# Kernel optimization log

Hardware: AMD Instinct MI355X
Metric: run time of the kernel (lower is better)

## Reference

```python
import jax, jax.numpy as jnp
import numpy as np
import math

D_MODEL = 512
NUM_HEADS = 8
B, L = 2, 4096
EPS_NORM = 1e-8
PLASTICITY = 1.0


def setup_inputs() -> dict:
    key = jax.random.key(0)
    ks = jax.random.split(key, 6)
    D, H = D_MODEL, NUM_HEADS
    std = 1.0 / math.sqrt(D)
    x = jax.random.normal(ks[0], (B, L, D), dtype=jnp.float32)
    qkv_w = jax.random.normal(ks[1], (3 * D, D), dtype=jnp.float32) * std
    qkv_b = jnp.zeros((3 * D,), dtype=jnp.float32)
    out_w = jax.random.normal(ks[2], (D, D), dtype=jnp.float32) * std
    out_b = jnp.zeros((D,), dtype=jnp.float32)
    decay_w = jax.random.normal(ks[3], (H, D), dtype=jnp.float32) * 0.02
    decay_b = jnp.full((H,), 4.0, dtype=jnp.float32)
    norm_scale = jnp.ones((D,), dtype=jnp.float32)
    return {"x": x, "qkv_w": qkv_w, "qkv_b": qkv_b, "out_w": out_w,
            "out_b": out_b, "decay_w": decay_w, "decay_b": decay_b,
            "norm_scale": norm_scale}


def _hebbian_forward(x, qkv_w, qkv_b, out_w, out_b, decay_w, decay_b, norm_scale):
    Bsz, Lsz, D = x.shape
    H = NUM_HEADS
    E = D // H
    # QKV projection (torch Linear: y = x @ W.T + b)
    qkv = x @ qkv_w.T + qkv_b
    q, k, v = jnp.split(qkv, 3, axis=-1)
    q = q.reshape(Bsz, Lsz, H, E)
    k = k.reshape(Bsz, Lsz, H, E)
    v = v.reshape(Bsz, Lsz, H, E)
    # feature map: elu(x) + 1
    q = (jax.nn.elu(q) + 1.0) / math.sqrt(E)
    k = jax.nn.elu(k) + 1.0
    # input-dependent decay per head
    decay_logits = x @ decay_w.T + decay_b          # (B,L,H)
    lambdas = (0.9 + 0.1 * jax.nn.sigmoid(decay_logits)) * PLASTICITY
    log_lambdas = jnp.log(jnp.clip(lambdas, 1e-6))[..., None]   # (B,L,H,1)
    log_lambda_cum = jnp.clip(jnp.cumsum(log_lambdas, axis=1), -50.0, 50.0)
    decay_k = jnp.exp(-log_lambda_cum)
    decay_q = jnp.exp(log_lambda_cum)
    k_decayed = k * decay_k
    q_decayed = q * decay_q
    # outer-product memory state cumsum: (B,L,H,E,E)
    kv = jnp.einsum('blhe,blhf->blhef', k_decayed, v)
    memory_state = jnp.cumsum(kv, axis=1)
    k_sum_decayed = jnp.cumsum(k_decayed, axis=1)
    num = jnp.einsum('blhe,blhef->blhf', q_decayed, memory_state)
    den = jnp.einsum('blhe,blhe->blh', q_decayed, k_sum_decayed)[..., None] + 1e-6
    out = (num / den).reshape(Bsz, Lsz, D)
    out = out @ out_w.T + out_b
    # RMSNorm (dropout is identity in eval)
    rnorm = jax.lax.rsqrt(jnp.mean(out * out, axis=-1, keepdims=True) + EPS_NORM)
    return out * rnorm * norm_scale


def reference(x, qkv_w, qkv_b, out_w, out_b, decay_w, decay_b, norm_scale):
    return _hebbian_forward(x, qkv_w, qkv_b, out_w, out_b, decay_w, decay_b, norm_scale)
```

## Files before the change

### kernel.cpp

```cpp
#include <hip/hip_runtime.h>

typedef unsigned short u16;
typedef unsigned int u32;

#define B_ 2
#define L_ 4096
#define D_ 512
#define H_ 8
#define E_ 64
#define M_ (B_*L_)
#define TD (3*D_)
#define NCH (L_/64)
#define BH (B_*H_)

typedef short bf16x8 __attribute__((ext_vector_type(8)));
typedef float f32x4 __attribute__((ext_vector_type(4)));

__device__ __forceinline__ float bf2f(u16 u){ return __uint_as_float(((u32)u)<<16); }
__device__ __forceinline__ u16 f2bf(float f){
  u32 u = __float_as_uint(f);
  u32 r = u + 0x7FFFu + ((u>>16)&1u);
  return (u16)(r>>16);
}
__device__ __forceinline__ float elu1(float v){ return v>0.f ? v+1.f : __expf(v); }

__device__ __forceinline__ void async_ld16(const u16* g, u16* l){
  __builtin_amdgcn_global_load_lds(
      (const __attribute__((address_space(1))) void*)g,
      (__attribute__((address_space(3))) void*)l, 16, 0, 0);
}

__global__ __launch_bounds__(256) void decay_conv_kernel(const float* __restrict__ x,
    const float* __restrict__ dw, const float* __restrict__ db,
    const float* __restrict__ qw, const float* __restrict__ ow,
    float* __restrict__ ll, u16* __restrict__ xb,
    u16* __restrict__ qwb, u16* __restrict__ owb)
{
  int blk = blockIdx.x;
  if (blk < 2048){
    int wv = threadIdx.x>>6, lane = threadIdx.x&63;
    int m = blk*4 + wv;
    float xr[8];
    #pragma unroll
    for (int i=0;i<8;i++) xr[i] = x[(size_t)m*D_ + lane + 64*i];
    #pragma unroll
    for (int i=0;i<8;i++) xb[(size_t)m*D_ + lane + 64*i] = f2bf(xr[i]);
    int b = m >> 12, l = m & (L_-1);
    float acc8[8];
    #pragma unroll
    for (int h=0; h<8; h++){
      float a = 0.f;
      #pragma unroll
      for (int i=0;i<8;i++) a += xr[i]*dw[h*D_ + lane + 64*i];
      acc8[h] = a;
    }
    float s4[4];
    #pragma unroll
    for (int i=0;i<4;i++){
      float a = acc8[2*i], bb = acc8[2*i+1];
      bool odd = lane & 1;
      float keep = odd ? bb : a;
      float send = odd ? a : bb;
      s4[i] = keep + __shfl_xor(send, 1);
    }
    float s2[2];
    #pragma unroll
    for (int j=0;j<2;j++){
      float a = s4[2*j], bb = s4[2*j+1];
      bool sel = (lane>>1) & 1;
      float keep = sel ? bb : a;
      float send = sel ? a : bb;
      s2[j] = keep + __shfl_xor(send, 2);
    }
    float r;
    {
      bool sel = (lane>>2) & 1;
      float keep = sel ? s2[1] : s2[0];
      float send = sel ? s2[0] : s2[1];
      r = keep + __shfl_xor(send, 4);
    }
    r += __shfl_xor(r, 8);
    r += __shfl_xor(r, 16);
    r += __shfl_xor(r, 32);
    if (lane < 8){
      float z = r + db[lane];
      float lam = 0.9f + 0.1f/(1.f + __expf(-z));
      ll[((b*H_+lane)*L_) + l] = __logf(lam);
    }
  } else {
    int gid = (blk-2048)*256 + threadIdx.x;
    const float* src; u16* dst; int off;
    if (gid < 196608){ src = qw; dst = qwb; off = gid; }
    else { src = ow; dst = owb; off = gid - 196608; }
    float4 v = ((const float4*)src)[off];
    ushort4 o; o.x=f2bf(v.x); o.y=f2bf(v.y); o.z=f2bf(v.z); o.w=f2bf(v.w);
    ((ushort4*)dst)[off] = o;
  }
}

__global__ __launch_bounds__(256) void scan_kernel(const float* __restrict__ ll,
    float* __restrict__ cb)
{
  int bh = blockIdx.x, t = threadIdx.x;
  int lane = t & 63, wv = t >> 6;
  const float* p = ll + (size_t)bh*L_ + t*16;
  float s[16];
  #pragma unroll
  for (int q=0;q<4;q++){
    float4 v = *(const float4*)(p + q*4);
    s[q*4+0]=v.x; s[q*4+1]=v.y; s[q*4+2]=v.z; s[q*4+3]=v.w;
  }
  #pragma unroll
  for (int i=1;i<16;i++) s[i] += s[i-1];
  float tot = s[15];
  float ws = tot;
  #pragma unroll
  for (int off=1; off<64; off<<=1){
    float tmp = __shfl_up(ws, off);
    if (lane >= off) ws += tmp;
  }
  __shared__ float wsum[4];
  if (lane == 63) wsum[wv] = ws;
  __syncthreads();
  float base = 0.f;
  #pragma unroll
  for (int w2=0; w2<3; w2++) if (w2 < wv) base += wsum[w2];
  float ex = base + ws - tot;
  float* c = cb + (size_t)bh*L_ + t*16;
  #pragma unroll
  for (int i=0;i<16;i++) c[i] = fminf(50.f, fmaxf(-50.f, ex + s[i]));
}

template<bool OB>
__global__ __launch_bounds__(256) void gemm_mfma(const u16* __restrict__ A,
    const u16* __restrict__ W, const float* __restrict__ bias,
    void* __restrict__ Cv, int M, int N, int K)
{
  __shared__ u16 As[2][128*32];
  __shared__ u16 Bs[2][128*32];
  int n0 = blockIdx.x*128, m0 = blockIdx.y*128;
  int t = threadIdx.x, wave = t>>6, lane = t&63;
  int wm = (wave>>1)*64, wn = (wave&1)*64;
  f32x4 acc[4][4] = {};
  int srow = wave*32 + (lane>>2);
  int scol = (lane&3)*8;
  const u16* gA = A + (size_t)(m0+srow)*K + scol;
  const u16* gB = W + (size_t)(n0+srow)*K + scol;
  int q8 = (lane>>4)*8, r16 = lane&15;
  {
    u16* lA = As[0] + wave*1024;
    u16* lB = Bs[0] + wave*1024;
    async_ld16(gA,                lA);
    async_ld16(gA + 16*(size_t)K, lA + 512);
    async_ld16(gB,                lB);
    async_ld16(gB + 16*(size_t)K, lB + 512);
  }
  __syncthreads();
  int cur = 0;
  #pragma unroll 2
  for (int k0=0; k0<K; k0+=32){
    if (k0 + 32 < K){
      u16* lA = As[cur^1] + wave*1024;
      u16* lB = Bs[cur^1] + wave*1024;
      async_ld16(gA + k0+32,                lA);
      async_ld16(gA + k0+32 + 16*(size_t)K, lA + 512);
      async_ld16(gB + k0+32,                lB);
      async_ld16(gB + k0+32 + 16*(size_t)K, lB + 512);
    }
    bf16x8 af[4], bfr[4];
    #pragma unroll
    for (int i=0;i<4;i++) af[i]  = *(const bf16x8*)&As[cur][(wm + i*16 + r16)*32 + q8];
    #pragma unroll
    for (int j=0;j<4;j++) bfr[j] = *(const bf16x8*)&Bs[cur][(wn + j*16 + r16)*32 + q8];
    #pragma unroll
    for (int i=0;i<4;i++)
      #pragma unroll
      for (int j=0;j<4;j++)
        acc[i][j] = __builtin_amdgcn_mfma_f32_16x16x32_bf16(af[i], bfr[j], acc[i][j], 0,0,0);
    __syncthreads();
    cur ^= 1;
  }
  #pragma unroll
  for (int i=0;i<4;i++){
    int row = m0 + wm + i*16 + (lane>>4)*4;
    #pragma unroll
    for (int j=0;j<4;j++){
      int col = n0 + wn + j*16 + r16;
      float bv = bias[col];
      #pragma unroll
      for (int r=0;r<4;r++){
        float val = acc[i][j][r] + bv;
        if (OB) ((u16*)Cv)[(size_t)(row+r)*N + col] = f2bf(val);
        else    ((float*)Cv)[(size_t)(row+r)*N + col] = val;
      }
    }
  }
}

__global__ __launch_bounds__(256) void transform_sums_kernel(const u16* __restrict__ qkvb,
    const float* __restrict__ cb, u16* __restrict__ qc, u16* __restrict__ kc,
    u16* __restrict__ vtc, u16* __restrict__ Stc, float* __restrict__ ksc)
{
  int bid = blockIdx.x;
  int bh = bid >> 6, ch = bid & 63;
  int b = bh >> 3, h = bh & 7;
  __shared__ u16 Ks[64*72];
  __shared__ u16 Vs[64*72];
  __shared__ u16 Ktl[128*40];
  __shared__ u16 Vtl[128*40];
  __shared__ float ksr[256];
  int t = threadIdx.x;
  size_t mbase = (size_t)b*L_ + ch*64;
  #pragma unroll
  for (int i=0;i<2;i++){
    int idx = t + 256*i;
    int l = idx>>3, e0 = (idx&7)*8;
    int kh = e0>>5, ej = e0&31;
    float c = cb[(size_t)bh*L_ + ch*64 + l];
    float eqc = __expf(c)*0.125f, ekc = __expf(-c);
    const u16* src = qkvb + (mbase+l)*TD + h*64 + e0;
    union { uint4 v; u16 s[8]; } in, o;
    in.v = *(const uint4*)src;
    #pragma unroll
    for (int j=0;j<8;j++) o.s[j] = f2bf(elu1(bf2f(in.s[j]))*eqc);
    *(uint4*)(qc + ((size_t)bid*2 + kh)*2048 + l*32 + ej) = o.v;
    in.v = *(const uint4*)(src + D_);
    #pragma unroll
    for (int j=0;j<8;j++) o.s[j] = f2bf(elu1(bf2f(in.s[j]))*ekc);
    *(uint4*)(kc + ((size_t)bid*2 + kh)*2048 + l*32 + ej) = o.v;
    *(uint4*)&Ks[l*72+e0] = o.v;
    *(uint4*)&Vs[l*72+e0] = *(const uint4*)(src + 2*D_);
  }
  __syncthreads();
  int e = t & 63, jq = t >> 6;
  {
    u16 kv[16] __attribute__((aligned(16)));
    u16 vv[16] __attribute__((aligned(16)));
    float ksum = 0.f;
    #pragma unroll
    for (int jj=0;jj<16;jj++){
      int j = jq*16+jj;
      kv[jj] = Ks[j*72 + e];
      ksum += bf2f(kv[jj]);
      vv[jj] = Vs[j*72 + e];
    }
    int kh = jq>>1, jl = (jq&1)*16;
    u16* kt = &Ktl[(kh*64 + e)*40 + jl];
    u16* vt = &Vtl[(kh*64 + e)*40 + jl];
    *(uint4*)kt     = *(const uint4*)&kv[0];
    *(uint4*)(kt+8) = *(const uint4*)&kv[8];
    *(uint4*)vt     = *(const uint4*)&vv[0];
    *(uint4*)(vt+8) = *(const uint4*)&vv[8];
    ksr[t] = ksum;
  }
  __syncthreads();
  {
    int row = t>>1, c0 = (t&1)*16;
    *(uint4*)&vtc[(size_t)bid*4096 + row*32 + c0]     = *(const uint4*)&Vtl[row*40 + c0];
    *(uint4*)&vtc[(size_t)bid*4096 + row*32 + c0 + 8] = *(const uint4*)&Vtl[row*40 + c0 + 8];
  }
  int w = t>>6, lane = t&63;
  int r16 = lane & 15, q8 = (lane>>4)*8;
  bf16x8 av[2];
  #pragma unroll
  for (int kh=0;kh<2;kh++)
    av[kh] = *(const bf16x8*)&Vtl[(kh*64 + w*16 + r16)*40 + q8];
  f32x4 acc[4] = {};
  #pragma unroll
  for (int et=0;et<4;et++)
    #pragma unroll
    for (int kh=0;kh<2;kh++){
      bf16x8 bv = *(const bf16x8*)&Ktl[(kh*64 + et*16 + r16)*40 + q8];
      acc[et] = __builtin_amdgcn_mfma_f32_16x16x32_bf16(av[kh], bv, acc[et], 0,0,0);
    }
  #pragma unroll
  for (int et=0;et<4;et++){
    int eh = et>>1, el = (et&1)*16 + r16;
    #pragma unroll
    for (int r=0;r<4;r++){
      int f = w*16 + (lane>>4)*4 + r;
      Stc[((size_t)bid*2 + eh)*2048 + f*32 + el] = f2bf(acc[et][r]);
    }
  }
  if (t < 64) ksc[bid*64 + t] = ksr[t] + ksr[64+t] + ksr[128+t] + ksr[192+t];
}

__global__ __launch_bounds__(256) void chunk_prefix_kernel(u16* __restrict__ Stc,
    float* __restrict__ ksc)
{
  int blk = blockIdx.x, t = threadIdx.x;
  if (blk < 128){
    int gid = blk*256 + t;
    int bh = gid >> 11, e2 = gid & 2047;
    u32* p = (u32*)Stc + (size_t)bh*131072 + e2;
    float r0 = 0.f, r1 = 0.f;
    #pragma unroll 16
    for (int ch=0; ch<NCH; ch++){
      u32 v = p[ch*2048];
      float lo = bf2f((u16)(v & 0xffffu));
      float hi = bf2f((u16)(v >> 16));
      p[ch*2048] = (u32)f2bf(r0) | ((u32)f2bf(r1) << 16);
      r0 += lo; r1 += hi;
    }
  } else {
    int gid2 = (blk-128)*256 + t;
    int bh2 = gid2 >> 6, e = gid2 & 63;
    float* kp = ksc + bh2*4096 + e;
    float kr = 0.f;
    #pragma unroll 8
    for (int ch=0; ch<NCH; ch++){
      float v = kp[ch*64]; kp[ch*64] = kr; kr += v;
    }
  }
}

__global__ __launch_bounds__(256) void chunk_out_kernel(const u16* __restrict__ qc,
    const u16* __restrict__ kc, const u16* __restrict__ vtc,
    const u16* __restrict__ Stc, const float* __restrict__ ksc,
    u16* __restrict__ attn)
{
  int bid = blockIdx.x;
  int bh = bid >> 6, ch = bid & 63;
  int b = bh >> 3, h = bh & 7;
  __shared__ u16 KV[16384];
  __shared__ u16 Ab[4096];
  __shared__ float kp[64], den4[256], den[64];
  int t = threadIdx.x, w = t>>6, lane = t&63;
  size_t mbase = (size_t)b*L_ + ch*64;
  const u16* gsrc = (w==0) ? qc : (w==1) ? kc : (w==2) ? vtc : Stc;
  {
    const u16* gbase = gsrc + (size_t)bid*4096 + lane*8;
    #pragma unroll
    for (int q=0;q<8;q++)
      async_ld16(gbase + q*512, KV + w*4096 + q*512);
  }
  if (t < 64) kp[t] = ksc[bid*64 + t];
  __syncthreads();
  const u16* Qs   = KV;
  const u16* Kb_s = KV + 4096;
  const u16* Vt_s = KV + 8192;
  const u16* St_s = KV + 12288;
  int r16 = lane & 15, q8 = (lane>>4)*8;
  bf16x8 aq[2];
  #pragma unroll
  for (int eh=0;eh<2;eh++)
    aq[eh] = *(const bf16x8*)&Qs[(eh*64 + w*16 + r16)*32 + q8];
  f32x4 accA[4] = {};
  #pragma unroll
  for (int jt=0;jt<4;jt++)
    #pragma unroll
    for (int eh=0;eh<2;eh++){
      bf16x8 bv = *(const bf16x8*)&Kb_s[(eh*64 + jt*16 + r16)*32 + q8];
      accA[jt] = __builtin_amdgcn_mfma_f32_16x16x32_bf16(aq[eh], bv, accA[jt], 0,0,0);
    }
  int l4 = t>>2, q4 = t&3;
  float dkp = 0.f;
  {
    int eh = q4>>1, el0 = (q4&1)*16;
    bf16x8 x1 = *(const bf16x8*)&Qs[(eh*64 + l4)*32 + el0];
    bf16x8 x2 = *(const bf16x8*)&Qs[(eh*64 + l4)*32 + el0 + 8];
    #pragma unroll
    for (int i=0;i<8;i++)
      dkp += bf2f((u16)x1[i])*kp[q4*16+i] + bf2f((u16)x2[i])*kp[q4*16+8+i];
  }
  #pragma unroll
  for (int jt=0;jt<4;jt++)
    #pragma unroll
    for (int r=0;r<4;r++){
      int lr = w*16 + ((lane>>4)<<2) + r;
      int j  = jt*16 + r16;
      Ab[((jt>>1)*64 + lr)*32 + (jt&1)*16 + r16] = (j <= lr) ? f2bf(accA[jt][r]) : (u16)0;
    }
  __syncthreads();
  float dA = 0.f;
  {
    int jh2 = q4>>1, jl0 = (q4&1)*16;
    bf16x8 y1 = *(const bf16x8*)&Ab[(jh2*64 + l4)*32 + jl0];
    bf16x8 y2 = *(const bf16x8*)&Ab[(jh2*64 + l4)*32 + jl0 + 8];
    #pragma unroll
    for (int i=0;i<8;i++) dA += bf2f((u16)y1[i]) + bf2f((u16)y2[i]);
  }
  den4[t] = dkp + dA;
  __syncthreads();
  if (t < 64) den[t] = den4[t*4] + den4[t*4+1] + den4[t*4+2] + den4[t*4+3] + 1e-6f;
  bf16x8 aA[2];
  #pragma unroll
  for (int jh=0;jh<2;jh++)
    aA[jh] = *(const bf16x8*)&Ab[(jh*64 + w*16 + r16)*32 + q8];
  f32x4 acc[4] = {};
  #pragma unroll
  for (int ft=0;ft<4;ft++){
    #pragma unroll
    for (int jh=0;jh<2;jh++){
      bf16x8 bv = *(const bf16x8*)&Vt_s[(jh*64 + ft*16 + r16)*32 + q8];
      acc[ft] = __builtin_amdgcn_mfma_f32_16x16x32_bf16(aA[jh], bv, acc[ft], 0,0,0);
    }
    #pragma unroll
    for (int eh=0;eh<2;eh++){
      bf16x8 bv = *(const bf16x8*)&St_s[(eh*64 + ft*16 + r16)*32 + q8];
      acc[ft] = __builtin_amdgcn_mfma_f32_16x16x32_bf16(aq[eh], bv, acc[ft], 0,0,0);
    }
  }
  __syncthreads();
  float inv[4];
  #pragma unroll
  for (int r=0;r<4;r++) inv[r] = 1.f / den[w*16 + ((lane>>4)<<2) + r];
  #pragma unroll
  for (int ft=0;ft<4;ft++)
    #pragma unroll
    for (int r=0;r<4;r++){
      int lr = w*16 + ((lane>>4)<<2) + r;
      attn[(mbase + lr)*D_ + h*64 + ft*16 + r16] = f2bf(acc[ft][r]*inv[r]);
    }
}

__global__ __launch_bounds__(256) void gemm_rms_kernel(const u16* __restrict__ A,
    const u16* __restrict__ W, const float* __restrict__ bias,
    const float* __restrict__ gnorm, float* __restrict__ out)
{
  __shared__ u16 As[2][32*32];
  __shared__ u16 Bs[2][512*32];
  __shared__ float ssq_l[4][32];
  __shared__ float rinv_l[32];
  int m0 = blockIdx.x*32;
  int t = threadIdx.x, wave = t>>6, lane = t&63;
  int wn = wave*128;
  int r16 = lane&15, q8 = (lane>>4)*8;
  f32x4 acc[2][8] = {};
  int scol = (t&3)*8;
  const u16* gB = W + (size_t)(t>>2)*512 + scol;
  const u16* gA = A + (size_t)(m0 + (t>>2))*512 + scol;
  {
    if (wave < 2) async_ld16(gA, As[0] + wave*512);
    #pragma unroll
    for (int it=0; it<8; it++)
      async_ld16(gB + it*32768, Bs[0] + wave*512 + it*2048);
  }
  __syncthreads();
  int cur = 0;
  #pragma unroll 2
  for (int k0=0; k0<512; k0+=32){
    if (k0 < 480){
      if (wave < 2) async_ld16(gA + k0+32, As[cur^1] + wave*512);
      #pragma unroll
      for (int it=0; it<8; it++)
        async_ld16(gB + k0+32 + it*32768, Bs[cur^1] + wave*512 + it*2048);
    }
    bf16x8 af0 = *(const bf16x8*)&As[cur][r16*32 + q8];
    bf16x8 af1 = *(const bf16x8*)&As[cur][(16 + r16)*32 + q8];
    #pragma unroll
    for (int j=0;j<8;j++){
      bf16x8 bv = *(const bf16x8*)&Bs[cur][(wn + j*16 + r16)*32 + q8];
      acc[0][j] = __builtin_amdgcn_mfma_f32_16x16x32_bf16(af0, bv, acc[0][j], 0,0,0);
      acc[1][j] = __builtin_amdgcn_mfma_f32_16x16x32_bf16(af1, bv, acc[1][j], 0,0,0);
    }
    __syncthreads();
    cur ^= 1;
  }
  int g = lane>>4;
  float bv8[8], gv8[8];
  #pragma unroll
  for (int j=0;j<8;j++){ int col = wn + j*16 + r16; bv8[j] = bias[col]; gv8[j] = gnorm[col]; }
  float ssq[2][4] = {};
  #pragma unroll
  for (int i=0;i<2;i++)
    #pragma unroll
    for (int j=0;j<8;j++)
      #pragma unroll
      for (int r=0;r<4;r++){
        float v = acc[i][j][r] + bv8[j];
        acc[i][j][r] = v;
        ssq[i][r] += v*v;
      }
  #pragma unroll
  for (int off=1; off<16; off<<=1)
    #pragma unroll
    for (int i=0;i<2;i++)
      #pragma unroll
      for (int r=0;r<4;r++)
        ssq[i][r] += __shfl_xor(ssq[i][r], off);
  if (r16 == 0){
    #pragma unroll
    for (int i=0;i<2;i++)
      #pragma unroll
      for (int r=0;r<4;r++)
        ssq_l[wave][i*16 + g*4 + r] = ssq[i][r];
  }
  __syncthreads();
  if (t < 32)
    rinv_l[t] = rsqrtf((ssq_l[0][t]+ssq_l[1][t]+ssq_l[2][t]+ssq_l[3][t])*(1.f/512.f) + 1e-8f);
  __syncthreads();
  #pragma unroll
  for (int i=0;i<2;i++)
    #pragma unroll
    for (int r=0;r<4;r++){
      int row = m0 + i*16 + g*4 + r;
      float ri = rinv_l[i*16 + g*4 + r];
      #pragma unroll
      for (int j=0;j<8;j++)
        out[(size_t)row*512 + wn + j*16 + r16] = acc[i][j][r]*ri*gv8[j];
    }
}

extern "C" void kernel_launch(void* const* d_in, const int* in_sizes, int n_in,
                              void* d_out, int out_size, void* d_ws, size_t ws_size,
                              hipStream_t stream)
{
  const float* x     = (const float*)d_in[0];
  const float* w_qkv = (const float*)d_in[1];
  const float* b_qkv = (const float*)d_in[2];
  const float* w_out = (const float*)d_in[3];
  const float* b_out = (const float*)d_in[4];
  const float* w_dec = (const float*)d_in[5];
  const float* b_dec = (const float*)d_in[6];
  const float* gnorm = (const float*)d_in[7];
  float* out = (float*)d_out;

  char* ws = (char*)d_ws;
  u16*   qkvb = (u16*)(ws);
  u16*   qc   = (u16*)(ws + 25165824);
  u16*   kc   = (u16*)(ws + 33554432);
  u16*   vtc  = (u16*)(ws + 41943040);
  u16*   Stc  = (u16*)(ws + 50331648);
  float* ksc  = (float*)(ws + 58720256);
  float* ll   = (float*)(ws + 58982400);
  float* cb   = (float*)(ws + 59244544);
  u16*   xb   = (u16*)(ws + 59506688);
  u16*   qwb  = (u16*)(ws + 67895296);
  u16*   owb  = (u16*)(ws + 69468160);
  u16*   attn = xb;

  decay_conv_kernel<<<dim3(3072), dim3(256), 0, stream>>>(x, w_dec, b_dec, w_qkv, w_out,
                                                          ll, xb, qwb, owb);
  scan_kernel<<<dim3(BH), dim3(256), 0, stream>>>(ll, cb);
  gemm_mfma<true><<<dim3(TD/128, M_/128), dim3(256), 0, stream>>>(xb, qwb, b_qkv, qkvb, M_, TD, D_);
  transform_sums_kernel<<<dim3(BH*NCH), dim3(256), 0, stream>>>(qkvb, cb, qc, kc, vtc, Stc, ksc);
  chunk_prefix_kernel<<<dim3(132), dim3(256), 0, stream>>>(Stc, ksc);
  chunk_out_kernel<<<dim3(BH*NCH), dim3(256), 0, stream>>>(qc, kc, vtc, Stc, ksc, attn);
  gemm_rms_kernel<<<dim3(M_/32), dim3(256), 0, stream>>>(attn, owb, b_out, gnorm, out);
}
```

Measured before the change: 156.0 us.

## Fuse QKV feature map and decay into GEMM epilogue, drop qkv buffer

The QKV GEMM epilogue now applies elu+1 and the exponential decay scaling and writes q, k and v directly into the chunked layout. This removes the intermediate qkv round trip through global memory and the transform pass. The V transpose moves into chunk_sums and chunk_out, which now transpose V in shared memory. Q fragments are read straight from global memory. The cost is scattered 2-byte stores in the GEMM epilogue and redundant V transposes in two kernels.

```diff
diff --git a/kernel.cpp b/kernel.cpp
--- a/kernel.cpp
+++ b/kernel.cpp
@@ -131,13 +131,14 @@
   for (int i=0;i<16;i++) c[i] = fminf(50.f, fmaxf(-50.f, ex + s[i]));
 }
 
-template<bool OB>
-__global__ __launch_bounds__(256) void gemm_mfma(const u16* __restrict__ A,
+__global__ __launch_bounds__(256) void gemm_qkv_fused(const u16* __restrict__ A,
     const u16* __restrict__ W, const float* __restrict__ bias,
-    void* __restrict__ Cv, int M, int N, int K)
+    const float* __restrict__ cb,
+    u16* __restrict__ qc, u16* __restrict__ kc, u16* __restrict__ vc)
 {
   __shared__ u16 As[2][128*32];
   __shared__ u16 Bs[2][128*32];
+  const int K = 512;
   int n0 = blockIdx.x*128, m0 = blockIdx.y*128;
   int t = threadIdx.x, wave = t>>6, lane = t&63;
   int wm = (wave>>1)*64, wn = (wave&1)*64;
@@ -180,56 +181,53 @@
     __syncthreads();
     cur ^= 1;
   }
+  int g = lane>>4;
+  int sec = n0 >> 9;
   #pragma unroll
   for (int i=0;i<4;i++){
-    int row = m0 + wm + i*16 + (lane>>4)*4;
+    int rowb = m0 + wm + i*16 + g*4;
     #pragma unroll
     for (int j=0;j<4;j++){
       int col = n0 + wn + j*16 + r16;
       float bv = bias[col];
+      int nn = col & 511, h2 = nn>>6, e = nn&63;
+      int bh2 = ((rowb>>12)<<3) | h2;
       #pragma unroll
       for (int r=0;r<4;r++){
+        int row = rowb + r;
         float val = acc[i][j][r] + bv;
-        if (OB) ((u16*)Cv)[(size_t)(row+r)*N + col] = f2bf(val);
-        else    ((float*)Cv)[(size_t)(row+r)*N + col] = val;
+        int l6 = row & 63, ch = (row>>6)&63;
+        int bid = (bh2<<6) | ch;
+        size_t a = ((size_t)(bid*2 + (e>>5)))*2048 + (size_t)l6*32 + (e&31);
+        if (sec == 0){
+          float c = cb[((size_t)bh2<<12) | (row & 4095)];
+          qc[a] = f2bf(elu1(val)*__expf(c)*0.125f);
+        } else if (sec == 1){
+          float c = cb[((size_t)bh2<<12) | (row & 4095)];
+          kc[a] = f2bf(elu1(val)*__expf(-c));
+        } else {
+          vc[a] = f2bf(val);
+        }
       }
     }
   }
 }
 
-__global__ __launch_bounds__(256) void transform_sums_kernel(const u16* __restrict__ qkvb,
-    const float* __restrict__ cb, u16* __restrict__ qc, u16* __restrict__ kc,
-    u16* __restrict__ vtc, u16* __restrict__ Stc, float* __restrict__ ksc)
+__global__ __launch_bounds__(256) void chunk_sums_kernel(const u16* __restrict__ kc,
+    const u16* __restrict__ vc, u16* __restrict__ Stc, float* __restrict__ ksc)
 {
   int bid = blockIdx.x;
-  int bh = bid >> 6, ch = bid & 63;
-  int b = bh >> 3, h = bh & 7;
-  __shared__ u16 Ks[64*72];
-  __shared__ u16 Vs[64*72];
-  __shared__ u16 Ktl[128*40];
-  __shared__ u16 Vtl[128*40];
+  __shared__ u16 Kc[4096], Vc[4096];
+  __shared__ u16 Ktl[5120], Vtl[5120];
   __shared__ float ksr[256];
-  int t = threadIdx.x;
-  size_t mbase = (size_t)b*L_ + ch*64;
-  #pragma unroll
-  for (int i=0;i<2;i++){
-    int idx = t + 256*i;
-    int l = idx>>3, e0 = (idx&7)*8;
-    int kh = e0>>5, ej = e0&31;
-    float c = cb[(size_t)bh*L_ + ch*64 + l];
-    float eqc = __expf(c)*0.125f, ekc = __expf(-c);
-    const u16* src = qkvb + (mbase+l)*TD + h*64 + e0;
-    union { uint4 v; u16 s[8]; } in, o;
-    in.v = *(const uint4*)src;
-    #pragma unroll
-    for (int j=0;j<8;j++) o.s[j] = f2bf(elu1(bf2f(in.s[j]))*eqc);
-    *(uint4*)(qc + ((size_t)bid*2 + kh)*2048 + l*32 + ej) = o.v;
-    in.v = *(const uint4*)(src + D_);
-    #pragma unroll
-    for (int j=0;j<8;j++) o.s[j] = f2bf(elu1(bf2f(in.s[j]))*ekc);
-    *(uint4*)(kc + ((size_t)bid*2 + kh)*2048 + l*32 + ej) = o.v;
-    *(uint4*)&Ks[l*72+e0] = o.v;
-    *(uint4*)&Vs[l*72+e0] = *(const uint4*)(src + 2*D_);
+  int t = threadIdx.x, w = t>>6, lane = t&63;
+  {
+    const u16* gk = kc + (size_t)bid*4096 + w*1024 + lane*8;
+    const u16* gv = vc + (size_t)bid*4096 + w*1024 + lane*8;
+    async_ld16(gk,       Kc + w*1024);
+    async_ld16(gk + 512, Kc + w*1024 + 512);
+    async_ld16(gv,       Vc + w*1024);
+    async_ld16(gv + 512, Vc + w*1024 + 512);
   }
   __syncthreads();
   int e = t & 63, jq = t >> 6;
@@ -240,13 +238,13 @@
     #pragma unroll
     for (int jj=0;jj<16;jj++){
       int j = jq*16+jj;
-      kv[jj] = Ks[j*72 + e];
+      kv[jj] = Kc[(e>>5)*2048 + j*32 + (e&31)];
       ksum += bf2f(kv[jj]);
-      vv[jj] = Vs[j*72 + e];
-    }
-    int kh = jq>>1, jl = (jq&1)*16;
-    u16* kt = &Ktl[(kh*64 + e)*40 + jl];
-    u16* vt = &Vtl[(kh*64 + e)*40 + jl];
+      vv[jj] = Vc[(e>>5)*2048 + j*32 + (e&31)];
+    }
+    int kh2 = jq>>1, jl = (jq&1)*16;
+    u16* kt = &Ktl[(kh2*64 + e)*40 + jl];
+    u16* vt = &Vtl[(kh2*64 + e)*40 + jl];
     *(uint4*)kt     = *(const uint4*)&kv[0];
     *(uint4*)(kt+8) = *(const uint4*)&kv[8];
     *(uint4*)vt     = *(const uint4*)&vv[0];
@@ -254,12 +252,6 @@
     ksr[t] = ksum;
   }
   __syncthreads();
-  {
-    int row = t>>1, c0 = (t&1)*16;
-    *(uint4*)&vtc[(size_t)bid*4096 + row*32 + c0]     = *(const uint4*)&Vtl[row*40 + c0];
-    *(uint4*)&vtc[(size_t)bid*4096 + row*32 + c0 + 8] = *(const uint4*)&Vtl[row*40 + c0 + 8];
-  }
-  int w = t>>6, lane = t&63;
   int r16 = lane & 15, q8 = (lane>>4)*8;
   bf16x8 av[2];
   #pragma unroll
@@ -315,54 +307,70 @@
 }
 
 __global__ __launch_bounds__(256) void chunk_out_kernel(const u16* __restrict__ qc,
-    const u16* __restrict__ kc, const u16* __restrict__ vtc,
+    const u16* __restrict__ kc, const u16* __restrict__ vc,
     const u16* __restrict__ Stc, const float* __restrict__ ksc,
     u16* __restrict__ attn)
 {
   int bid = blockIdx.x;
   int bh = bid >> 6, ch = bid & 63;
   int b = bh >> 3, h = bh & 7;
-  __shared__ u16 KV[16384];
+  __shared__ u16 Kb_l[4096];
+  __shared__ u16 Vc_l[4096];
+  __shared__ u16 St_l[4096];
+  __shared__ u16 Vt[5120];
   __shared__ u16 Ab[4096];
-  __shared__ float kp[64], den4[256], den[64];
+  __shared__ float R2[320];
   int t = threadIdx.x, w = t>>6, lane = t&63;
   size_t mbase = (size_t)b*L_ + ch*64;
-  const u16* gsrc = (w==0) ? qc : (w==1) ? kc : (w==2) ? vtc : Stc;
-  {
-    const u16* gbase = gsrc + (size_t)bid*4096 + lane*8;
-    #pragma unroll
-    for (int q=0;q<8;q++)
-      async_ld16(gbase + q*512, KV + w*4096 + q*512);
-  }
-  if (t < 64) kp[t] = ksc[bid*64 + t];
-  __syncthreads();
-  const u16* Qs   = KV;
-  const u16* Kb_s = KV + 4096;
-  const u16* Vt_s = KV + 8192;
-  const u16* St_s = KV + 12288;
+  {
+    const u16* gk = kc  + (size_t)bid*4096 + w*1024 + lane*8;
+    const u16* gv = vc  + (size_t)bid*4096 + w*1024 + lane*8;
+    const u16* gs = Stc + (size_t)bid*4096 + w*1024 + lane*8;
+    async_ld16(gk,       Kb_l + w*1024);
+    async_ld16(gk + 512, Kb_l + w*1024 + 512);
+    async_ld16(gv,       Vc_l + w*1024);
+    async_ld16(gv + 512, Vc_l + w*1024 + 512);
+    async_ld16(gs,       St_l + w*1024);
+    async_ld16(gs + 512, St_l + w*1024 + 512);
+  }
   int r16 = lane & 15, q8 = (lane>>4)*8;
+  const u16* qg = qc + (size_t)bid*4096;
   bf16x8 aq[2];
   #pragma unroll
   for (int eh=0;eh<2;eh++)
-    aq[eh] = *(const bf16x8*)&Qs[(eh*64 + w*16 + r16)*32 + q8];
+    aq[eh] = *(const bf16x8*)(qg + eh*2048 + (w*16 + r16)*32 + q8);
+  int l4 = t>>2, q4 = t&3;
+  int ehd = q4>>1, el0 = (q4&1)*16;
+  bf16x8 x1 = *(const bf16x8*)(qg + ehd*2048 + l4*32 + el0);
+  bf16x8 x2 = *(const bf16x8*)(qg + ehd*2048 + l4*32 + el0 + 8);
+  union { float4 v[4]; float f[16]; } kp;
+  #pragma unroll
+  for (int qq=0;qq<4;qq++)
+    kp.v[qq] = *(const float4*)(ksc + bid*64 + q4*16 + qq*4);
+  __syncthreads();
+  {
+    int e = t & 63, jq = t >> 6;
+    u16 vv[16] __attribute__((aligned(16)));
+    #pragma unroll
+    for (int jj=0;jj<16;jj++)
+      vv[jj] = Vc_l[(e>>5)*2048 + (jq*16+jj)*32 + (e&31)];
+    int jh = jq>>1, jl = (jq&1)*16;
+    u16* vt = &Vt[(jh*64 + e)*40 + jl];
+    *(uint4*)vt     = *(const uint4*)&vv[0];
+    *(uint4*)(vt+8) = *(const uint4*)&vv[8];
+  }
   f32x4 accA[4] = {};
   #pragma unroll
   for (int jt=0;jt<4;jt++)
     #pragma unroll
     for (int eh=0;eh<2;eh++){
-      bf16x8 bv = *(const bf16x8*)&Kb_s[(eh*64 + jt*16 + r16)*32 + q8];
+      bf16x8 bv = *(const bf16x8*)&Kb_l[(eh*64 + jt*16 + r16)*32 + q8];
       accA[jt] = __builtin_amdgcn_mfma_f32_16x16x32_bf16(aq[eh], bv, accA[jt], 0,0,0);
     }
-  int l4 = t>>2, q4 = t&3;
   float dkp = 0.f;
-  {
-    int eh = q4>>1, el0 = (q4&1)*16;
-    bf16x8 x1 = *(const bf16x8*)&Qs[(eh*64 + l4)*32 + el0];
-    bf16x8 x2 = *(const bf16x8*)&Qs[(eh*64 + l4)*32 + el0 + 8];
-    #pragma unroll
-    for (int i=0;i<8;i++)
-      dkp += bf2f((u16)x1[i])*kp[q4*16+i] + bf2f((u16)x2[i])*kp[q4*16+8+i];
-  }
+  #pragma unroll
+  for (int i=0;i<8;i++)
+    dkp += bf2f((u16)x1[i])*kp.f[i] + bf2f((u16)x2[i])*kp.f[8+i];
   #pragma unroll
   for (int jt=0;jt<4;jt++)
     #pragma unroll
@@ -380,9 +388,9 @@
     #pragma unroll
     for (int i=0;i<8;i++) dA += bf2f((u16)y1[i]) + bf2f((u16)y2[i]);
   }
-  den4[t] = dkp + dA;
-  __syncthreads();
-  if (t < 64) den[t] = den4[t*4] + den4[t*4+1] + den4[t*4+2] + den4[t*4+3] + 1e-6f;
+  R2[t] = dkp + dA;
+  __syncthreads();
+  if (t < 64) R2[256+t] = R2[t*4] + R2[t*4+1] + R2[t*4+2] + R2[t*4+3] + 1e-6f;
   bf16x8 aA[2];
   #pragma unroll
   for (int jh=0;jh<2;jh++)
@@ -392,19 +400,19 @@
   for (int ft=0;ft<4;ft++){
     #pragma unroll
     for (int jh=0;jh<2;jh++){
-      bf16x8 bv = *(const bf16x8*)&Vt_s[(jh*64 + ft*16 + r16)*32 + q8];
+      bf16x8 bv = *(const bf16x8*)&Vt[(jh*64 + ft*16 + r16)*40 + q8];
       acc[ft] = __builtin_amdgcn_mfma_f32_16x16x32_bf16(aA[jh], bv, acc[ft], 0,0,0);
     }
     #pragma unroll
     for (int eh=0;eh<2;eh++){
-      bf16x8 bv = *(const bf16x8*)&St_s[(eh*64 + ft*16 + r16)*32 + q8];
+      bf16x8 bv = *(const bf16x8*)&St_l[(eh*64 + ft*16 + r16)*32 + q8];
       acc[ft] = __builtin_amdgcn_mfma_f32_16x16x32_bf16(aq[eh], bv, acc[ft], 0,0,0);
     }
   }
   __syncthreads();
   float inv[4];
   #pragma unroll
-  for (int r=0;r<4;r++) inv[r] = 1.f / den[w*16 + ((lane>>4)<<2) + r];
+  for (int r=0;r<4;r++) inv[r] = 1.f / R2[256 + w*16 + ((lane>>4)<<2) + r];
   #pragma unroll
   for (int ft=0;ft<4;ft++)
     #pragma unroll
@@ -517,25 +525,24 @@
   float* out = (float*)d_out;
 
   char* ws = (char*)d_ws;
-  u16*   qkvb = (u16*)(ws);
-  u16*   qc   = (u16*)(ws + 25165824);
-  u16*   kc   = (u16*)(ws + 33554432);
-  u16*   vtc  = (u16*)(ws + 41943040);
-  u16*   Stc  = (u16*)(ws + 50331648);
-  float* ksc  = (float*)(ws + 58720256);
-  float* ll   = (float*)(ws + 58982400);
-  float* cb   = (float*)(ws + 59244544);
-  u16*   xb   = (u16*)(ws + 59506688);
-  u16*   qwb  = (u16*)(ws + 67895296);
-  u16*   owb  = (u16*)(ws + 69468160);
+  u16*   qc   = (u16*)(ws);
+  u16*   kc   = (u16*)(ws + 8388608);
+  u16*   vc   = (u16*)(ws + 16777216);
+  u16*   Stc  = (u16*)(ws + 25165824);
+  float* ksc  = (float*)(ws + 33554432);
+  float* ll   = (float*)(ws + 33816576);
+  float* cb   = (float*)(ws + 34078720);
+  u16*   xb   = (u16*)(ws + 34340864);
+  u16*   qwb  = (u16*)(ws + 42729472);
+  u16*   owb  = (u16*)(ws + 44302336);
   u16*   attn = xb;
 
   decay_conv_kernel<<<dim3(3072), dim3(256), 0, stream>>>(x, w_dec, b_dec, w_qkv, w_out,
                                                           ll, xb, qwb, owb);
   scan_kernel<<<dim3(BH), dim3(256), 0, stream>>>(ll, cb);
-  gemm_mfma<true><<<dim3(TD/128, M_/128), dim3(256), 0, stream>>>(xb, qwb, b_qkv, qkvb, M_, TD, D_);
-  transform_sums_kernel<<<dim3(BH*NCH), dim3(256), 0, stream>>>(qkvb, cb, qc, kc, vtc, Stc, ksc);
+  gemm_qkv_fused<<<dim3(TD/128, M_/128), dim3(256), 0, stream>>>(xb, qwb, b_qkv, cb, qc, kc, vc);
+  chunk_sums_kernel<<<dim3(BH*NCH), dim3(256), 0, stream>>>(kc, vc, Stc, ksc);
   chunk_prefix_kernel<<<dim3(132), dim3(256), 0, stream>>>(Stc, ksc);
-  chunk_out_kernel<<<dim3(BH*NCH), dim3(256), 0, stream>>>(qc, kc, vtc, Stc, ksc, attn);
+  chunk_out_kernel<<<dim3(BH*NCH), dim3(256), 0, stream>>>(qc, kc, vc, Stc, ksc, attn);
   gemm_rms_kernel<<<dim3(M_/32), dim3(256), 0, stream>>>(attn, owb, b_out, gnorm, out);
 }
```

New measurement: 162.7 us. 1.04x slower.
